# Optimization experiments

Hardware: AMD Instinct MI355X
Metric: run time of the kernel (lower is better)

The kernel has to match this reference:

```python
import jax, jax.numpy as jnp
import numpy as np

TAU = 0.1

def _conv(x, w, padding):
    return jax.lax.conv_general_dilated(
        x, w, window_strides=(1, 1), padding=padding,
        dimension_numbers=("NCHW", "OIHW", "NCHW"))


def _bilinear_border(img, gx, gy):
    # img: (H,W). gx,gy: (H,W) normalized coords in [-1,1].
    # Matches torch grid_sample(mode='bilinear', align_corners=True, padding_mode='border').
    H, W = img.shape
    px = jnp.clip((gx + 1.0) * 0.5 * (W - 1), 0.0, W - 1)  # border: clamp coord
    py = jnp.clip((gy + 1.0) * 0.5 * (H - 1), 0.0, H - 1)
    x0 = jnp.floor(px)
    y0 = jnp.floor(py)
    wx = px - x0
    wy = py - y0
    x0i = x0.astype(jnp.int32)
    y0i = y0.astype(jnp.int32)
    x1i = jnp.minimum(x0i + 1, W - 1)
    y1i = jnp.minimum(y0i + 1, H - 1)
    v00 = img[y0i, x0i]
    v01 = img[y0i, x1i]
    v10 = img[y1i, x0i]
    v11 = img[y1i, x1i]
    top = v00 * (1.0 - wx) + v01 * wx
    bot = v10 * (1.0 - wx) + v11 * wx
    return top * (1.0 - wy) + bot * wy

_sample = jax.vmap(_bilinear_border)  # over flattened B*C axis


def setup_inputs() -> dict:
    key = jax.random.key(0)
    k1, k2, k3, k4 = jax.random.split(key, 4)
    B, C, H, W = 8, 64, 192, 192
    SH = 8
    x = jax.random.normal(k1, (B, C, H, W), dtype=jnp.float32)
    # kaiming_normal * 0.1 scale on first conv
    w1 = jax.random.normal(k2, (SH, C, 3, 3), dtype=jnp.float32) * (np.sqrt(2.0 / (C * 9)) * 0.1)
    # original zero-inits w2; use small random values for a nontrivial reference
    w2 = jax.random.normal(k3, (4 * C, SH, 1, 1), dtype=jnp.float32) * 0.02
    b2 = jax.random.normal(k4, (4 * C,), dtype=jnp.float32) * 0.5
    log_scale = jnp.asarray(np.log(0.1), dtype=jnp.float32)
    return {"x": x, "w1": w1, "w2": w2, "b2": b2, "log_scale": log_scale}


def reference(x, w1, w2, b2, log_scale):
    B, C, H, W = x.shape
    h = jax.nn.gelu(_conv(x, w1, "SAME"), approximate=False)
    coeffs = _conv(h, w2, "VALID") + b2[None, :, None, None]  # (B,4C,H,W)
    coeffs = coeffs.reshape(B, C, 4, H, W)  # channel = c*4 + k, as in torch .view
    a = jax.nn.softplus(coeffs[:, :, 0])
    bx = coeffs[:, :, 1]
    by = coeffs[:, :, 2]
    c = jnp.clip(coeffs[:, :, 3], -5.0, 5.0)
    s = jnp.sqrt(a * TAU + 1e-8).reshape(B * C, H, W)
    dx = (bx * TAU).reshape(B * C, H, W)
    dy = (by * TAU).reshape(B * C, H, W)
    bgx = jnp.broadcast_to(jnp.linspace(-1.0, 1.0, W, dtype=x.dtype)[None, :], (H, W))[None]
    bgy = jnp.broadcast_to(jnp.linspace(-1.0, 1.0, H, dtype=x.dtype)[:, None], (H, W))[None]
    xf = x.reshape(B * C, H, W)
    u_px = _sample(xf, bgx + s + dx, bgy + dy)
    u_nx = _sample(xf, bgx - s + dx, bgy + dy)
    u_py = _sample(xf, bgx + dx, bgy + s + dy)
    u_ny = _sample(xf, bgx + dx, bgy - s + dy)
    evolution = (0.25 * (u_px + u_nx + u_py + u_ny)).reshape(B, C, H, W)
    return jnp.exp(log_scale) * (evolution + TAU * c * x)
```

## Files before the change

kernel.cpp:

```cpp
#include <hip/hip_runtime.h>

#define HH 192
#define WW 192
#define CC 64
#define BB 8
#define SH 8
#define HWSZ (HH*WW)
#define TAU 0.1f

__global__ __launch_bounds__(256) void transpose_w1_kernel(
    const float* __restrict__ w1, float* __restrict__ wt)
{
    int i = blockIdx.x * 256 + threadIdx.x;
    if (i < CC * SH * 9) {
        int c  = i / (SH * 9);
        int r  = i - c * (SH * 9);
        int sh = r / 9;
        int k  = r - sh * 9;
        wt[i] = w1[((size_t)sh * CC + c) * 9 + k];
    }
}

__global__ __launch_bounds__(256) void conv1_gelu_kernel(
    const float* __restrict__ x, const float* __restrict__ wt, float* __restrict__ h)
{
    const int li  = blockIdx.x;
    const int b   = li & 7;
    const int m   = li >> 3;
    const int tyb = m / 12, txb = m - tyb * 12;

    const int t  = threadIdx.x;
    const int tx = t & 15, ty = t >> 4;
    const int xo = txb * 16 + tx;
    const int yo = tyb * 16 + ty;
    const int pix = yo * WW + xo;

    const float* xb = x + (size_t)b * CC * HWSZ;

    float acc[SH];
#pragma unroll
    for (int sh = 0; sh < SH; sh++) acc[sh] = 0.f;

    const bool border = (txb == 0) | (txb == 11) | (tyb == 0) | (tyb == 11);

    if (!border) {
        const float* p = xb + pix;
        for (int c = 0; c < CC; c++) {
            const float* pc = p + (size_t)c * HWSZ;
            float v[9];
            v[0] = pc[-WW - 1]; v[1] = pc[-WW]; v[2] = pc[-WW + 1];
            v[3] = pc[-1];      v[4] = pc[0];   v[5] = pc[1];
            v[6] = pc[WW - 1];  v[7] = pc[WW];  v[8] = pc[WW + 1];
            const float* ws = wt + c * (SH * 9);
#pragma unroll
            for (int sh = 0; sh < SH; sh++) {
                float a = acc[sh];
#pragma unroll
                for (int k = 0; k < 9; k++) a = fmaf(v[k], ws[sh * 9 + k], a);
                acc[sh] = a;
            }
        }
    } else {
        const int ym1 = max(yo - 1, 0), yp1 = min(yo + 1, HH - 1);
        const int xm1 = max(xo - 1, 0), xp1 = min(xo + 1, WW - 1);
        const int r0 = ym1 * WW, r1 = yo * WW, r2 = yp1 * WW;
        const bool vy0 = yo > 0, vy2 = yo < HH - 1, vx0 = xo > 0, vx2 = xo < WW - 1;
        int  o[9]  = {r0 + xm1, r0 + xo, r0 + xp1,
                      r1 + xm1, r1 + xo, r1 + xp1,
                      r2 + xm1, r2 + xo, r2 + xp1};
        bool mk[9] = {vy0 && vx0, vy0, vy0 && vx2,
                      vx0,        true, vx2,
                      vy2 && vx0, vy2, vy2 && vx2};
        for (int c = 0; c < CC; c++) {
            const float* pc = xb + (size_t)c * HWSZ;
            float v[9];
#pragma unroll
            for (int k = 0; k < 9; k++) v[k] = pc[o[k]];
#pragma unroll
            for (int k = 0; k < 9; k++) if (!mk[k]) v[k] = 0.f;
            const float* ws = wt + c * (SH * 9);
#pragma unroll
            for (int sh = 0; sh < SH; sh++) {
                float a = acc[sh];
#pragma unroll
                for (int k = 0; k < 9; k++) a = fmaf(v[k], ws[sh * 9 + k], a);
                acc[sh] = a;
            }
        }
    }

    float g[SH];
#pragma unroll
    for (int sh = 0; sh < SH; sh++)
        g[sh] = 0.5f * acc[sh] * (1.f + erff(acc[sh] * 0.70710678118654752f));
    float4 o0, o1;
    o0.x = g[0]; o0.y = g[1]; o0.z = g[2]; o0.w = g[3];
    o1.x = g[4]; o1.y = g[5]; o1.z = g[6]; o1.w = g[7];
    float4* hp = (float4*)&h[((size_t)b * HWSZ + pix) * SH];
    hp[0] = o0;
    hp[1] = o1;
}

#define TILES_PER_PLANE 144
#define NPLANES (BB*CC)

__global__ __launch_bounds__(256) void coeff_sample_kernel(
    const float* __restrict__ x, const float* __restrict__ hbuf,
    const float* __restrict__ w2, const float* __restrict__ b2,
    const float* __restrict__ log_scale, float* __restrict__ out)
{
    const int li = blockIdx.x;
    const int rr = li & 7;
    const int m  = li >> 3;
    const int q  = m / TILES_PER_PLANE;
    const int tt = m - q * TILES_PER_PLANE;
    const int bc = (q << 3) | rr;
    const int tyb = tt / 12, txb = tt - tyb * 12;

    const int t  = threadIdx.x;
    const int tx = t & 15;
    const int ty = t >> 4;
    const int xo = txb * 16 + tx;
    const int y  = tyb * 16 + ty;
    const int c  = bc & 63;
    const int pix = y * WW + xo;

    const float4* hp4 = (const float4*)&hbuf[((size_t)(bc >> 6) * HWSZ + pix) * SH];
    float4 h0 = hp4[0], h1 = hp4[1];
    float hk[SH] = {h0.x, h0.y, h0.z, h0.w, h1.x, h1.y, h1.z, h1.w};

    const int c4 = c * 4;
    float coeff[4];
#pragma unroll
    for (int j = 0; j < 4; j++) {
        const float* wr = w2 + (size_t)(c4 + j) * SH;
        float s = b2[c4 + j];
#pragma unroll
        for (int k = 0; k < SH; k++) s = fmaf(hk[k], wr[k], s);
        coeff[j] = s;
    }

    float z  = coeff[0];
    float a  = fmaxf(z, 0.f) + __logf(1.f + __expf(-fabsf(z)));
    float s  = __builtin_amdgcn_sqrtf(fmaf(a, TAU, 1e-8f));
    float dx = coeff[1] * TAU;
    float dy = coeff[2] * TAU;
    float cc = __builtin_amdgcn_fmed3f(coeff[3], -5.f, 5.f);

    const float* img = x + (size_t)bc * HWSZ;
    const float px0 = (float)xo + dx * 95.5f;
    const float py0 = (float)y  + dy * 95.5f;
    const float sp  = s * 95.5f;

    float u;
    {
        float pyc = __builtin_amdgcn_fmed3f(py0, 0.f, 191.f);
        float y0f = floorf(pyc);
        float wy  = pyc - y0f;
        int y0 = (int)y0f;
        unsigned r0 = (unsigned)(y0 * WW);
        unsigned r1 = r0 + ((y0 < HH - 1) ? WW : 0);
        u = 0.f;
#pragma unroll
        for (int sgn = 0; sgn < 2; sgn++) {
            float px  = sgn ? (px0 - sp) : (px0 + sp);
            float pxc = __builtin_amdgcn_fmed3f(px, 0.f, 191.f);
            float x0f = floorf(pxc);
            float wx  = pxc - x0f;
            int  x0 = (int)x0f;
            bool hi = x0 > WW - 2;
            unsigned xc = (unsigned)min(x0, WW - 2);
            float2 t0 = *(const float2*)(img + (r0 + xc));
            float2 t1 = *(const float2*)(img + (r1 + xc));
            float v00 = hi ? t0.y : t0.x;
            float v10 = hi ? t1.y : t1.x;
            float top = fmaf(wx, t0.y - v00, v00);
            float bot = fmaf(wx, t1.y - v10, v10);
            u += fmaf(wy, bot - top, top);
        }
    }
    {
        float pxc = __builtin_amdgcn_fmed3f(px0, 0.f, 191.f);
        float x0f = floorf(pxc);
        float wx  = pxc - x0f;
        int  x0 = (int)x0f;
        bool hi = x0 > WW - 2;
        unsigned xc = (unsigned)min(x0, WW - 2);
#pragma unroll
        for (int sgn = 0; sgn < 2; sgn++) {
            float py  = sgn ? (py0 - sp) : (py0 + sp);
            float pyc = __builtin_amdgcn_fmed3f(py, 0.f, 191.f);
            float y0f = floorf(pyc);
            float wy  = pyc - y0f;
            int y0 = (int)y0f;
            unsigned r0 = (unsigned)(y0 * WW);
            unsigned r1 = r0 + ((y0 < HH - 1) ? WW : 0);
            float2 t0 = *(const float2*)(img + (r0 + xc));
            float2 t1 = *(const float2*)(img + (r1 + xc));
            float v00 = hi ? t0.y : t0.x;
            float v10 = hi ? t1.y : t1.x;
            float top = fmaf(wx, t0.y - v00, v00);
            float bot = fmaf(wx, t1.y - v10, v10);
            u += fmaf(wy, bot - top, top);
        }
    }

    float xv    = img[(unsigned)pix];
    float scale = __expf(log_scale[0]);
    out[(size_t)bc * HWSZ + pix] = scale * fmaf(0.25f, u, TAU * cc * xv);
}

extern "C" void kernel_launch(void* const* d_in, const int* in_sizes, int n_in,
                              void* d_out, int out_size, void* d_ws, size_t ws_size,
                              hipStream_t stream)
{
    const float* x   = (const float*)d_in[0];
    const float* w1  = (const float*)d_in[1];
    const float* w2  = (const float*)d_in[2];
    const float* b2  = (const float*)d_in[3];
    const float* ls  = (const float*)d_in[4];
    float* out = (float*)d_out;
    float* h   = (float*)d_ws;

    float* wt = out + (size_t)out_size - CC * SH * 9;

    dim3 blk(256);
    transpose_w1_kernel<<<dim3((CC * SH * 9 + 255) / 256), blk, 0, stream>>>(w1, wt);

    conv1_gelu_kernel<<<dim3(12 * 12 * BB), blk, 0, stream>>>(x, wt, h);

    coeff_sample_kernel<<<dim3(NPLANES * TILES_PER_PLANE), blk, 0, stream>>>(
        x, h, w2, b2, ls, out);
}
```

Before: 280.4 us.

## Fuse conv1+GELU with coefficient and sampling into one per-pixel kernel

Merges the conv/GELU kernel and the coefficient/sampling kernel so each thread keeps its 8 hidden activations in registers and loops over all 64 channels to compute coefficients, do the four bilinear samples and write the output. This removes the intermediate h buffer write and read and one kernel launch. In exchange the grid shrinks from tens of thousands of blocks to 1152. Each thread serially performs 64 channels of gather loads, which can reduce latency hiding and parallelism.

Result: faster. 273.0 us (-2.6%).

```diff
diff --git a/kernel.cpp b/kernel.cpp
--- a/kernel.cpp
+++ b/kernel.cpp
@@ -21,8 +21,10 @@
     }
 }
 
-__global__ __launch_bounds__(256) void conv1_gelu_kernel(
-    const float* __restrict__ x, const float* __restrict__ wt, float* __restrict__ h)
+__global__ __launch_bounds__(256) void fused_kernel(
+    const float* __restrict__ x, const float* __restrict__ wt,
+    const float* __restrict__ w2, const float* __restrict__ b2,
+    const float* __restrict__ log_scale, float* __restrict__ out)
 {
     const int li  = blockIdx.x;
     const int b   = li & 7;
@@ -89,125 +91,95 @@
         }
     }
 
-    float g[SH];
+    float hk[SH];
 #pragma unroll
     for (int sh = 0; sh < SH; sh++)
-        g[sh] = 0.5f * acc[sh] * (1.f + erff(acc[sh] * 0.70710678118654752f));
-    float4 o0, o1;
-    o0.x = g[0]; o0.y = g[1]; o0.z = g[2]; o0.w = g[3];
-    o1.x = g[4]; o1.y = g[5]; o1.z = g[6]; o1.w = g[7];
-    float4* hp = (float4*)&h[((size_t)b * HWSZ + pix) * SH];
-    hp[0] = o0;
-    hp[1] = o1;
-}
-
-#define TILES_PER_PLANE 144
-#define NPLANES (BB*CC)
-
-__global__ __launch_bounds__(256) void coeff_sample_kernel(
-    const float* __restrict__ x, const float* __restrict__ hbuf,
-    const float* __restrict__ w2, const float* __restrict__ b2,
-    const float* __restrict__ log_scale, float* __restrict__ out)
-{
-    const int li = blockIdx.x;
-    const int rr = li & 7;
-    const int m  = li >> 3;
-    const int q  = m / TILES_PER_PLANE;
-    const int tt = m - q * TILES_PER_PLANE;
-    const int bc = (q << 3) | rr;
-    const int tyb = tt / 12, txb = tt - tyb * 12;
-
-    const int t  = threadIdx.x;
-    const int tx = t & 15;
-    const int ty = t >> 4;
-    const int xo = txb * 16 + tx;
-    const int y  = tyb * 16 + ty;
-    const int c  = bc & 63;
-    const int pix = y * WW + xo;
-
-    const float4* hp4 = (const float4*)&hbuf[((size_t)(bc >> 6) * HWSZ + pix) * SH];
-    float4 h0 = hp4[0], h1 = hp4[1];
-    float hk[SH] = {h0.x, h0.y, h0.z, h0.w, h1.x, h1.y, h1.z, h1.w};
-
-    const int c4 = c * 4;
-    float coeff[4];
-#pragma unroll
-    for (int j = 0; j < 4; j++) {
-        const float* wr = w2 + (size_t)(c4 + j) * SH;
-        float s = b2[c4 + j];
-#pragma unroll
-        for (int k = 0; k < SH; k++) s = fmaf(hk[k], wr[k], s);
-        coeff[j] = s;
-    }
-
-    float z  = coeff[0];
-    float a  = fmaxf(z, 0.f) + __logf(1.f + __expf(-fabsf(z)));
-    float s  = __builtin_amdgcn_sqrtf(fmaf(a, TAU, 1e-8f));
-    float dx = coeff[1] * TAU;
-    float dy = coeff[2] * TAU;
-    float cc = __builtin_amdgcn_fmed3f(coeff[3], -5.f, 5.f);
-
-    const float* img = x + (size_t)bc * HWSZ;
-    const float px0 = (float)xo + dx * 95.5f;
-    const float py0 = (float)y  + dy * 95.5f;
-    const float sp  = s * 95.5f;
-
-    float u;
-    {
-        float pyc = __builtin_amdgcn_fmed3f(py0, 0.f, 191.f);
-        float y0f = floorf(pyc);
-        float wy  = pyc - y0f;
-        int y0 = (int)y0f;
-        unsigned r0 = (unsigned)(y0 * WW);
-        unsigned r1 = r0 + ((y0 < HH - 1) ? WW : 0);
-        u = 0.f;
-#pragma unroll
-        for (int sgn = 0; sgn < 2; sgn++) {
-            float px  = sgn ? (px0 - sp) : (px0 + sp);
-            float pxc = __builtin_amdgcn_fmed3f(px, 0.f, 191.f);
+        hk[sh] = 0.5f * acc[sh] * (1.f + erff(acc[sh] * 0.70710678118654752f));
+
+    const float scale = __expf(log_scale[0]);
+    const float xf = (float)xo, yf = (float)yo;
+    float* outp = out + (size_t)b * CC * HWSZ + pix;
+
+    for (int c = 0; c < CC; c++) {
+        const float* w2c = w2 + c * 32;
+        const float* b2c = b2 + c * 4;
+        float coeff[4];
+#pragma unroll
+        for (int j = 0; j < 4; j++) {
+            float s = b2c[j];
+#pragma unroll
+            for (int k = 0; k < SH; k++) s = fmaf(hk[k], w2c[j * 8 + k], s);
+            coeff[j] = s;
+        }
+
+        float z  = coeff[0];
+        float a  = fmaxf(z, 0.f) + __logf(1.f + __expf(-fabsf(z)));
+        float s  = __builtin_amdgcn_sqrtf(fmaf(a, TAU, 1e-8f));
+        float dx = coeff[1] * TAU;
+        float dy = coeff[2] * TAU;
+        float cc = __builtin_amdgcn_fmed3f(coeff[3], -5.f, 5.f);
+
+        const float* img = xb + (size_t)c * HWSZ;
+        const float px0 = xf + dx * 95.5f;
+        const float py0 = yf + dy * 95.5f;
+        const float sp  = s * 95.5f;
+
+        float u;
+        {
+            float pyc = __builtin_amdgcn_fmed3f(py0, 0.f, 191.f);
+            float y0f = floorf(pyc);
+            float wy  = pyc - y0f;
+            int y0 = (int)y0f;
+            unsigned r0 = (unsigned)(y0 * WW);
+            unsigned r1 = r0 + ((y0 < HH - 1) ? WW : 0);
+            u = 0.f;
+#pragma unroll
+            for (int sgn = 0; sgn < 2; sgn++) {
+                float px  = sgn ? (px0 - sp) : (px0 + sp);
+                float pxc = __builtin_amdgcn_fmed3f(px, 0.f, 191.f);
+                float x0f = floorf(pxc);
+                float wx  = pxc - x0f;
+                int  x0 = (int)x0f;
+                bool hi = x0 > WW - 2;
+                unsigned xc = (unsigned)min(x0, WW - 2);
+                float2 t0 = *(const float2*)(img + (r0 + xc));
+                float2 t1 = *(const float2*)(img + (r1 + xc));
+                float v00 = hi ? t0.y : t0.x;
+                float v10 = hi ? t1.y : t1.x;
+                float top = fmaf(wx, t0.y - v00, v00);
+                float bot = fmaf(wx, t1.y - v10, v10);
+                u += fmaf(wy, bot - top, top);
+            }
+        }
+        {
+            float pxc = __builtin_amdgcn_fmed3f(px0, 0.f, 191.f);
             float x0f = floorf(pxc);
             float wx  = pxc - x0f;
             int  x0 = (int)x0f;
             bool hi = x0 > WW - 2;
             unsigned xc = (unsigned)min(x0, WW - 2);
-            float2 t0 = *(const float2*)(img + (r0 + xc));
-            float2 t1 = *(const float2*)(img + (r1 + xc));
-            float v00 = hi ? t0.y : t0.x;
-            float v10 = hi ? t1.y : t1.x;
-            float top = fmaf(wx, t0.y - v00, v00);
-            float bot = fmaf(wx, t1.y - v10, v10);
-            u += fmaf(wy, bot - top, top);
-        }
+#pragma unroll
+            for (int sgn = 0; sgn < 2; sgn++) {
+                float py  = sgn ? (py0 - sp) : (py0 + sp);
+                float pyc = __builtin_amdgcn_fmed3f(py, 0.f, 191.f);
+                float y0f = floorf(pyc);
+                float wy  = pyc - y0f;
+                int y0 = (int)y0f;
+                unsigned r0 = (unsigned)(y0 * WW);
+                unsigned r1 = r0 + ((y0 < HH - 1) ? WW : 0);
+                float2 t0 = *(const float2*)(img + (r0 + xc));
+                float2 t1 = *(const float2*)(img + (r1 + xc));
+                float v00 = hi ? t0.y : t0.x;
+                float v10 = hi ? t1.y : t1.x;
+                float top = fmaf(wx, t0.y - v00, v00);
+                float bot = fmaf(wx, t1.y - v10, v10);
+                u += fmaf(wy, bot - top, top);
+            }
+        }
+
+        float xv = img[(unsigned)pix];
+        outp[(size_t)c * HWSZ] = scale * fmaf(0.25f, u, TAU * cc * xv);
     }
-    {
-        float pxc = __builtin_amdgcn_fmed3f(px0, 0.f, 191.f);
-        float x0f = floorf(pxc);
-        float wx  = pxc - x0f;
-        int  x0 = (int)x0f;
-        bool hi = x0 > WW - 2;
-        unsigned xc = (unsigned)min(x0, WW - 2);
-#pragma unroll
-        for (int sgn = 0; sgn < 2; sgn++) {
-            float py  = sgn ? (py0 - sp) : (py0 + sp);
-            float pyc = __builtin_amdgcn_fmed3f(py, 0.f, 191.f);
-            float y0f = floorf(pyc);
-            float wy  = pyc - y0f;
-            int y0 = (int)y0f;
-            unsigned r0 = (unsigned)(y0 * WW);
-            unsigned r1 = r0 + ((y0 < HH - 1) ? WW : 0);
-            float2 t0 = *(const float2*)(img + (r0 + xc));
-            float2 t1 = *(const float2*)(img + (r1 + xc));
-            float v00 = hi ? t0.y : t0.x;
-            float v10 = hi ? t1.y : t1.x;
-            float top = fmaf(wx, t0.y - v00, v00);
-            float bot = fmaf(wx, t1.y - v10, v10);
-            u += fmaf(wy, bot - top, top);
-        }
-    }
-
-    float xv    = img[(unsigned)pix];
-    float scale = __expf(log_scale[0]);
-    out[(size_t)bc * HWSZ + pix] = scale * fmaf(0.25f, u, TAU * cc * xv);
 }
 
 extern "C" void kernel_launch(void* const* d_in, const int* in_sizes, int n_in,
@@ -220,15 +192,10 @@
     const float* b2  = (const float*)d_in[3];
     const float* ls  = (const float*)d_in[4];
     float* out = (float*)d_out;
-    float* h   = (float*)d_ws;
-
-    float* wt = out + (size_t)out_size - CC * SH * 9;
+    float* wt  = (float*)d_ws;
 
     dim3 blk(256);
     transpose_w1_kernel<<<dim3((CC * SH * 9 + 255) / 256), blk, 0, stream>>>(w1, wt);
 
-    conv1_gelu_kernel<<<dim3(12 * 12 * BB), blk, 0, stream>>>(x, wt, h);
-
-    coeff_sample_kernel<<<dim3(NPLANES * TILES_PER_PLANE), blk, 0, stream>>>(
-        x, h, w2, b2, ls, out);
+    fused_kernel<<<dim3(12 * 12 * BB), blk, 0, stream>>>(x, wt, w2, b2, ls, out);
 }
```
